# Kernel tuning notes

Measured on AMD Instinct MI355X. Metric: run time of the kernel, lower is better.

The kernel has to match this reference:

```python
import jax, jax.numpy as jnp
import numpy as np

N_NODES = 50000
N_EDGES = 800000
D_IN = 128
H1 = H2 = H3 = 128
N_CLASS = 16
N_GRAPHS = 500


def setup_inputs() -> dict:
    key = jax.random.key(0)
    ks = jax.random.split(key, 10)
    x = jax.random.normal(ks[0], (N_NODES, D_IN), dtype=jnp.float32)
    edge_src = jax.random.randint(ks[1], (N_EDGES,), 0, N_NODES)
    edge_dst = jax.random.randint(ks[2], (N_EDGES,), 0, N_NODES)
    idx = jnp.sort(jax.random.randint(ks[3], (N_NODES,), 0, N_GRAPHS))
    s = 0.02  # small init scale
    W1 = jax.random.normal(ks[4], (D_IN, H1), dtype=jnp.float32) * s
    W2 = jax.random.normal(ks[5], (H1, H2), dtype=jnp.float32) * s
    W3 = jax.random.normal(ks[6], (H2, H3), dtype=jnp.float32) * s
    W4 = jax.random.normal(ks[7], (H3, N_CLASS), dtype=jnp.float32) * s
    b1 = jnp.zeros((H1,), jnp.float32)
    b2 = jnp.zeros((H2,), jnp.float32)
    b3 = jnp.zeros((H3,), jnp.float32)
    b4 = jnp.zeros((N_CLASS,), jnp.float32)
    return {"x": x, "edge_src": edge_src, "edge_dst": edge_dst, "idx": idx,
            "W1": W1, "b1": b1, "W2": W2, "b2": b2,
            "W3": W3, "b3": b3, "W4": W4, "b4": b4}


def reference(x, edge_src, edge_dst, idx, W1, b1, W2, b2, W3, b3, W4, b4):
    # adj_tilde @ h  with binary adjacency + identity, in edge-list form:
    # row i accumulates h[j] for every edge (i<-j), plus h[i] from the eye.
    def propagate(h):
        return h + jax.ops.segment_sum(h[edge_src], edge_dst, num_segments=h.shape[0])

    z1 = jax.nn.relu(propagate(x) @ W1 + b1)            # [N, H1]
    h = propagate(z1) @ W2 + b2                          # [N, H2]
    # scatter_add pooling per graph id (fixed number of graphs for jit)
    pooled = jax.ops.segment_sum(h, idx, num_segments=N_GRAPHS)  # [G, H2]
    zg = jax.nn.relu(pooled @ W3 + b3)                   # [G, H3]
    out = zg @ W4 + b4                                   # [G, C]
    return jax.nn.log_softmax(out, axis=1)
```

## Files before the change

kernel.cpp:

```cpp
#include <hip/hip_runtime.h>
#include <hip/hip_bf16.h>
#include <math.h>

#define NN 50000
#define NE 800000
#define DD 128
#define NG 500
#define NC 16

#define BBITS 6
#define BDSTS 64
#define NBK ((NN + BDSTS - 1) / BDSTS)
#define NCHUNK 256
#define EPB (NE / NCHUNK)
#define ECAP 1536
#define NSLICE 4

using short8 = __attribute__((ext_vector_type(8))) short;
using f32x4  = __attribute__((ext_vector_type(4))) float;

static __device__ __forceinline__ ushort f2bf(float f) {
    __hip_bfloat16 h = __float2bfloat16(f);
    ushort r;
    __builtin_memcpy(&r, &h, sizeof(r));
    return r;
}
static __device__ __forceinline__ float bflo(uint v) { return __uint_as_float(v << 16); }
static __device__ __forceinline__ float bfhi(uint v) { return __uint_as_float(v & 0xffff0000u); }
static __device__ __forceinline__ uint packbf(float lo, float hi) {
    return ((uint)f2bf(hi) << 16) | (uint)f2bf(lo);
}

static __device__ __forceinline__ void add8(float* acc, uint4 v) {
    acc[0] += bflo(v.x); acc[1] += bfhi(v.x);
    acc[2] += bflo(v.y); acc[3] += bfhi(v.y);
    acc[4] += bflo(v.z); acc[5] += bfhi(v.z);
    acc[6] += bflo(v.w); acc[7] += bfhi(v.w);
}

static __device__ __forceinline__ int lower_bound_idx(const int* __restrict__ idx, int g) {
    if (g >= NG) return NN;
    int lo = 0, hi = NN;
    while (lo < hi) {
        int mid = (lo + hi) >> 1;
        if (idx[mid] < g) lo = mid + 1; else hi = mid;
    }
    return lo;
}

static __device__ __forceinline__ int chunk_of_block(int blk) {
    return (blk & 7) * 32 + (blk >> 3);
}

__global__ __launch_bounds__(256) void csr_count_kernel(const int* __restrict__ edst,
                                                        int* __restrict__ cnt) {
    __shared__ int hist[NBK];
    int t = threadIdx.x;
    int chunk = chunk_of_block(blockIdx.x);
    const int e0 = chunk * EPB;
    for (int b = t; b < NBK; b += 256) hist[b] = 0;
    __syncthreads();
    for (int i = t; i < EPB; i += 256) atomicAdd(&hist[edst[e0 + i] >> BBITS], 1);
    __syncthreads();
    for (int b = t; b < NBK; b += 256) cnt[(size_t)chunk * NBK + b] = hist[b];
}

__global__ __launch_bounds__(256) void csr_scan1_kernel(const int* __restrict__ cnt,
                                                        int* __restrict__ bpos,
                                                        int* __restrict__ btot) {
    __shared__ int s[256];
    int b = blockIdx.x, t = threadIdx.x;
    int v = cnt[(size_t)t * NBK + b];
    s[t] = v;
    __syncthreads();
    for (int d = 1; d < 256; d <<= 1) {
        int x = (t >= d) ? s[t - d] : 0;
        __syncthreads();
        s[t] += x;
        __syncthreads();
    }
    bpos[b * NCHUNK + t] = s[t] - v;
    if (t == 255) btot[b] = s[255];
}

__global__ __launch_bounds__(1024) void csr_scan2_kernel(const int* __restrict__ btot,
                                                         int* __restrict__ bbase) {
    __shared__ int s[1024];
    int t = threadIdx.x;
    int v = (t < NBK) ? btot[t] : 0;
    s[t] = v;
    __syncthreads();
    for (int d = 1; d < 1024; d <<= 1) {
        int x = (t >= d) ? s[t - d] : 0;
        __syncthreads();
        s[t] += x;
        __syncthreads();
    }
    if (t < NBK) bbase[t] = s[t] - v;
}

__global__ __launch_bounds__(256) void csr_scatter_kernel(const int* __restrict__ esrc,
                                                          const int* __restrict__ edst,
                                                          const int* __restrict__ bbase,
                                                          const int* __restrict__ bpos,
                                                          uint* __restrict__ baux) {
    __shared__ int lbase[NBK];
    __shared__ int cur[NBK];
    int t = threadIdx.x;
    int chunk = chunk_of_block(blockIdx.x);
    const int e0 = chunk * EPB;
    for (int b = t; b < NBK; b += 256) {
        lbase[b] = bbase[b] + bpos[b * NCHUNK + chunk];
        cur[b] = 0;
    }
    __syncthreads();
    for (int i = t; i < EPB; i += 256) {
        int d = edst[e0 + i], s = esrc[e0 + i];
        int b = d >> BBITS;
        int r = atomicAdd(&cur[b], 1);
        baux[lbase[b] + r] = ((uint)(d & (BDSTS - 1)) << 16) | (uint)s;
    }
}

__global__ __launch_bounds__(256) void bucket_sort_kernel(const uint* __restrict__ baux,
                                                          const int* __restrict__ btot,
                                                          const int* __restrict__ bbase,
                                                          int* __restrict__ offsets,
                                                          ushort* __restrict__ csr) {
    __shared__ uint ent[ECAP];
    __shared__ int hist[BDSTS], lofs[BDSTS], cur[BDSTS];
    int b = blockIdx.x, t = threadIdx.x;
    int n = btot[b];
    int base = bbase[b];
    if (t < BDSTS) hist[t] = 0;
    __syncthreads();
    for (int i = t; i < n; i += 256) {
        uint e = baux[base + i];
        ent[i] = e;
        atomicAdd(&hist[e >> 16], 1);
    }
    __syncthreads();
    if (t < BDSTS) lofs[t] = hist[t];
    __syncthreads();
    for (int d = 1; d < BDSTS; d <<= 1) {
        int x = 0;
        if (t < BDSTS && t >= d) x = lofs[t - d];
        __syncthreads();
        if (t < BDSTS) lofs[t] += x;
        __syncthreads();
    }
    int d0 = b * BDSTS;
    if (t < BDSTS) {
        int excl = lofs[t] - hist[t];
        lofs[t] = excl;
        cur[t] = 0;
        if (d0 + t < NN) offsets[d0 + t] = base + excl;
    }
    if (b == NBK - 1 && t == 0) offsets[NN] = NE;
    __syncthreads();
    for (int i = t; i < n; i += 256) {
        uint e = ent[i];
        int j = e >> 16;
        int pos = base + lofs[j] + atomicAdd(&cur[j], 1);
        csr[pos] = (ushort)(e & 0xffffu);
    }
}

__global__ void convert_w1t_kernel(const float* __restrict__ W1, ushort* __restrict__ W1t) {
    int flat = blockIdx.x * 256 + threadIdx.x;
    if (flat < 128 * 128) {
        int k = flat >> 7, n = flat & 127;
        W1t[n * 128 + k] = f2bf(W1[flat]);
    }
}

__global__ __launch_bounds__(256) void gemm_mfma_kernel(const float* __restrict__ X,
                                                        const ushort* __restrict__ W1t,
                                                        ushort* __restrict__ Y, int M) {
    const int tid = threadIdx.x;
    const int wave = tid >> 6, lane = tid & 63;
    const int wm = wave >> 1, wn = wave & 1;
    const int m0 = blockIdx.x * 128 + wm * 64;
    const int n0 = wn * 64;
    const int lr = lane & 15;
    const int lk = (lane >> 4) * 8;

    int rows[4];
    bool valid[4];
    #pragma unroll
    for (int m = 0; m < 4; ++m) {
        rows[m] = m0 + m * 16 + lr;
        valid[m] = rows[m] < M;
    }

    f32x4 acc[4][4] = {};

    #pragma unroll
    for (int kc = 0; kc < 4; ++kc) {
        const int kb = kc * 32 + lk;
        short8 a[4];
        #pragma unroll
        for (int m = 0; m < 4; ++m) {
            union { short8 v; ushort u[8]; } ua;
            if (valid[m]) {
                const float* p = &X[(size_t)rows[m] * 128 + kb];
                float4 v0 = *reinterpret_cast<const float4*>(p);
                float4 v1 = *reinterpret_cast<const float4*>(p + 4);
                ua.u[0] = f2bf(v0.x); ua.u[1] = f2bf(v0.y);
                ua.u[2] = f2bf(v0.z); ua.u[3] = f2bf(v0.w);
                ua.u[4] = f2bf(v1.x); ua.u[5] = f2bf(v1.y);
                ua.u[6] = f2bf(v1.z); ua.u[7] = f2bf(v1.w);
            } else {
                #pragma unroll
                for (int j = 0; j < 8; ++j) ua.u[j] = 0;
            }
            a[m] = ua.v;
        }
        short8 b[4];
        #pragma unroll
        for (int n = 0; n < 4; ++n) {
            b[n] = *reinterpret_cast<const short8*>(&W1t[(size_t)(n0 + n * 16 + lr) * 128 + kb]);
        }
        #pragma unroll
        for (int m = 0; m < 4; ++m)
            #pragma unroll
            for (int n = 0; n < 4; ++n)
                acc[m][n] = __builtin_amdgcn_mfma_f32_16x16x32_bf16(a[m], b[n], acc[m][n], 0, 0, 0);
    }

    const int rbase = (lane >> 4) * 4;
    #pragma unroll
    for (int m = 0; m < 4; ++m) {
        #pragma unroll
        for (int r = 0; r < 4; ++r) {
            int row = m0 + m * 16 + rbase + r;
            if (row < M) {
                #pragma unroll
                for (int n = 0; n < 4; ++n) {
                    Y[(size_t)row * 128 + n0 + n * 16 + lr] = f2bf(acc[m][n][r]);
                }
            }
        }
    }
}

__global__ __launch_bounds__(256) void prop1_kernel(const ushort* __restrict__ In,
                                                    const int* __restrict__ offs,
                                                    const ushort* __restrict__ csr,
                                                    const float* __restrict__ bias,
                                                    ushort* __restrict__ Out, int n) {
    int node = (blockIdx.x * blockDim.x + threadIdx.x) >> 6;
    int lane = threadIdx.x & 63;
    if (node >= n) return;
    const int q = lane >> 4;
    const int p = lane & 15;
    const uint4* Ir = reinterpret_cast<const uint4*>(In);

    float acc[8] = {};
    if (q == 0) add8(acc, Ir[(size_t)node * 16 + p]);

    int e = offs[node] + q, e1 = offs[node + 1];
    for (; e + 12 < e1; e += 16) {
        int s0 = csr[e], s1 = csr[e + 4], s2 = csr[e + 8], s3 = csr[e + 12];
        uint4 v0 = Ir[(size_t)s0 * 16 + p];
        uint4 v1 = Ir[(size_t)s1 * 16 + p];
        uint4 v2 = Ir[(size_t)s2 * 16 + p];
        uint4 v3 = Ir[(size_t)s3 * 16 + p];
        add8(acc, v0); add8(acc, v1); add8(acc, v2); add8(acc, v3);
    }
    for (; e < e1; e += 4) add8(acc, Ir[(size_t)csr[e] * 16 + p]);

    #pragma unroll
    for (int j = 0; j < 8; ++j) {
        acc[j] += __shfl_xor(acc[j], 16);
        acc[j] += __shfl_xor(acc[j], 32);
    }

    if (q == 0) {
        float4 bA = *reinterpret_cast<const float4*>(&bias[p * 8]);
        float4 bB = *reinterpret_cast<const float4*>(&bias[p * 8 + 4]);
        uint4 o;
        o.x = packbf(fmaxf(acc[0] + bA.x, 0.f), fmaxf(acc[1] + bA.y, 0.f));
        o.y = packbf(fmaxf(acc[2] + bA.z, 0.f), fmaxf(acc[3] + bA.w, 0.f));
        o.z = packbf(fmaxf(acc[4] + bB.x, 0.f), fmaxf(acc[5] + bB.y, 0.f));
        o.w = packbf(fmaxf(acc[6] + bB.z, 0.f), fmaxf(acc[7] + bB.w, 0.f));
        reinterpret_cast<uint4*>(Out)[(size_t)node * 16 + p] = o;
    }
}

__global__ __launch_bounds__(256) void prop2pool_kernel(const ushort* __restrict__ Z1,
                                                        const int* __restrict__ offs,
                                                        const ushort* __restrict__ csr,
                                                        const int* __restrict__ idx,
                                                        float* __restrict__ partials) {
    int g = blockIdx.x >> 2, s = blockIdx.x & (NSLICE - 1);
    int gs = lower_bound_idx(idx, g);
    int ge = lower_bound_idx(idx, g + 1);
    int w = threadIdx.x >> 6, lane = threadIdx.x & 63;
    int q = lane >> 4, p = lane & 15;
    int stream = s * 16 + w * 4 + q;
    const uint4* Zr = reinterpret_cast<const uint4*>(Z1);

    float acc[8] = {};
    for (int i = gs + stream; i < ge; i += 64) add8(acc, Zr[(size_t)i * 16 + p]);
    int E0 = offs[gs], E1 = offs[ge];
    int e = E0 + stream;
    for (; e + 64 < E1; e += 128) {
        int s0 = csr[e], s1 = csr[e + 64];
        uint4 v0 = Zr[(size_t)s0 * 16 + p];
        uint4 v1 = Zr[(size_t)s1 * 16 + p];
        add8(acc, v0); add8(acc, v1);
    }
    if (e < E1) add8(acc, Zr[(size_t)csr[e] * 16 + p]);

    #pragma unroll
    for (int j = 0; j < 8; ++j) {
        acc[j] += __shfl_xor(acc[j], 16);
        acc[j] += __shfl_xor(acc[j], 32);
    }
    __shared__ float red[4][128];
    if (q == 0) {
        #pragma unroll
        for (int j = 0; j < 8; ++j) red[w][p * 8 + j] = acc[j];
    }
    __syncthreads();
    int t = threadIdx.x;
    if (t < 128) {
        partials[((size_t)g * NSLICE + s) * 128 + t] =
            red[0][t] + red[1][t] + red[2][t] + red[3][t];
    }
}

__global__ __launch_bounds__(128) void head_kernel(const float* __restrict__ partials,
                                                   const int* __restrict__ idx,
                                                   const float* __restrict__ W2, const float* __restrict__ b2,
                                                   const float* __restrict__ W3, const float* __restrict__ b3,
                                                   const float* __restrict__ W4, const float* __restrict__ b4,
                                                   float* __restrict__ out) {
    int g = blockIdx.x, t = threadIdx.x;
    __shared__ float vs[128], hs[128], zs[128], os[16];
    const float* pp = &partials[(size_t)g * NSLICE * 128];
    vs[t] = pp[t] + pp[128 + t] + pp[256 + t] + pp[384 + t];
    __syncthreads();
    float c = (float)(lower_bound_idx(idx, g + 1) - lower_bound_idx(idx, g));
    float a = c * b2[t];
    #pragma unroll 8
    for (int k = 0; k < 128; ++k) a = fmaf(vs[k], W2[k * 128 + t], a);
    hs[t] = a;
    __syncthreads();
    float z = b3[t];
    #pragma unroll 8
    for (int k = 0; k < 128; ++k) z = fmaf(hs[k], W3[k * 128 + t], z);
    zs[t] = fmaxf(z, 0.f);
    __syncthreads();
    if (t < 16) {
        float oo = b4[t];
        #pragma unroll 8
        for (int k = 0; k < 128; ++k) oo = fmaf(zs[k], W4[k * 16 + t], oo);
        os[t] = oo;
    }
    __syncthreads();
    if (t < 16) {
        float m = -INFINITY;
        #pragma unroll
        for (int k = 0; k < 16; ++k) m = fmaxf(m, os[k]);
        float ssum = 0.f;
        #pragma unroll
        for (int k = 0; k < 16; ++k) ssum += expf(os[k] - m);
        out[g * 16 + t] = os[t] - m - logf(ssum);
    }
}

extern "C" void kernel_launch(void* const* d_in, const int* in_sizes, int n_in,
                              void* d_out, int out_size, void* d_ws, size_t ws_size,
                              hipStream_t stream) {
    const float* x    = (const float*)d_in[0];
    const int*   esrc = (const int*)d_in[1];
    const int*   edst = (const int*)d_in[2];
    const int*   idx  = (const int*)d_in[3];
    const float* W1   = (const float*)d_in[4];
    const float* b1   = (const float*)d_in[5];
    const float* W2   = (const float*)d_in[6];
    const float* b2   = (const float*)d_in[7];
    const float* W3   = (const float*)d_in[8];
    const float* b3   = (const float*)d_in[9];
    const float* W4   = (const float*)d_in[10];
    const float* b4   = (const float*)d_in[11];
    float* out = (float*)d_out;

    char* w = (char*)d_ws;
    auto alloc = [&](size_t bytes) -> void* {
        void* p = (void*)w;
        w += (bytes + 255) & ~(size_t)255;
        return p;
    };
    int* cnt      = (int*)alloc((size_t)NCHUNK * NBK * 4);
    int* bpos     = (int*)alloc((size_t)NBK * NCHUNK * 4);
    int* btot     = (int*)alloc((size_t)NBK * 4);
    int* bbase    = (int*)alloc((size_t)NBK * 4);
    uint* baux    = (uint*)alloc((size_t)NE * 4);
    int* offsets  = (int*)alloc((size_t)(NN + 1) * 4);
    ushort* csr   = (ushort*)alloc((size_t)NE * 2);
    ushort* w1t   = (ushort*)alloc((size_t)DD * DD * 2);
    ushort* y     = (ushort*)alloc((size_t)NN * DD * 2);
    ushort* z1    = (ushort*)alloc((size_t)NN * DD * 2);
    float* partials = (float*)alloc((size_t)NG * NSLICE * DD * 4);

    convert_w1t_kernel<<<64, 256, 0, stream>>>(W1, w1t);

    csr_count_kernel<<<NCHUNK, 256, 0, stream>>>(edst, cnt);
    csr_scan1_kernel<<<NBK, 256, 0, stream>>>(cnt, bpos, btot);
    csr_scan2_kernel<<<1, 1024, 0, stream>>>(btot, bbase);
    csr_scatter_kernel<<<NCHUNK, 256, 0, stream>>>(esrc, edst, bbase, bpos, baux);
    bucket_sort_kernel<<<NBK, 256, 0, stream>>>(baux, btot, bbase, offsets, csr);

    gemm_mfma_kernel<<<(NN + 127) / 128, 256, 0, stream>>>(x, w1t, y, NN);

    prop1_kernel<<<NN / 4, 256, 0, stream>>>(y, offsets, csr, b1, z1, NN);

    prop2pool_kernel<<<NG * NSLICE, 256, 0, stream>>>(z1, offsets, csr, idx, partials);

    head_kernel<<<NG, 128, 0, stream>>>(partials, idx, W2, b2, W3, b3, W4, b4, out);
}
```

Measured before the change: 135.1 us.

## Merge independent setup kernels into shared launches and unroll pooling gather

Independent setup stages now share launches: the W1 transpose/convert runs as extra blocks of the CSR count kernel, and the first GEMM runs as extra blocks of the per-bucket scan kernel. This removes two launches and lets the GEMM overlap with the CSR scan work. Separately, the prop2pool edge gather is unrolled from two to four outstanding loads per stream to raise memory-level parallelism. The cost is heterogeneous blocks in one grid, which can raise register and shared-memory pressure and lower occupancy for the fused kernels.

```diff
diff --git a/kernel.cpp b/kernel.cpp
--- a/kernel.cpp
+++ b/kernel.cpp
@@ -15,6 +15,7 @@
 #define EPB (NE / NCHUNK)
 #define ECAP 1536
 #define NSLICE 4
+#define GEMMBLK ((NN + 127) / 128)
 
 using short8 = __attribute__((ext_vector_type(8))) short;
 using f32x4  = __attribute__((ext_vector_type(4))) float;
@@ -52,135 +53,36 @@
     return (blk & 7) * 32 + (blk >> 3);
 }
 
-__global__ __launch_bounds__(256) void csr_count_kernel(const int* __restrict__ edst,
-                                                        int* __restrict__ cnt) {
-    __shared__ int hist[NBK];
+__global__ __launch_bounds__(256) void k0_count_convert_kernel(const int* __restrict__ edst,
+                                                               int* __restrict__ cnt,
+                                                               const float* __restrict__ W1,
+                                                               ushort* __restrict__ W1t) {
     int t = threadIdx.x;
-    int chunk = chunk_of_block(blockIdx.x);
-    const int e0 = chunk * EPB;
-    for (int b = t; b < NBK; b += 256) hist[b] = 0;
-    __syncthreads();
-    for (int i = t; i < EPB; i += 256) atomicAdd(&hist[edst[e0 + i] >> BBITS], 1);
-    __syncthreads();
-    for (int b = t; b < NBK; b += 256) cnt[(size_t)chunk * NBK + b] = hist[b];
-}
-
-__global__ __launch_bounds__(256) void csr_scan1_kernel(const int* __restrict__ cnt,
-                                                        int* __restrict__ bpos,
-                                                        int* __restrict__ btot) {
-    __shared__ int s[256];
-    int b = blockIdx.x, t = threadIdx.x;
-    int v = cnt[(size_t)t * NBK + b];
-    s[t] = v;
-    __syncthreads();
-    for (int d = 1; d < 256; d <<= 1) {
-        int x = (t >= d) ? s[t - d] : 0;
-        __syncthreads();
-        s[t] += x;
-        __syncthreads();
-    }
-    bpos[b * NCHUNK + t] = s[t] - v;
-    if (t == 255) btot[b] = s[255];
-}
-
-__global__ __launch_bounds__(1024) void csr_scan2_kernel(const int* __restrict__ btot,
-                                                         int* __restrict__ bbase) {
-    __shared__ int s[1024];
-    int t = threadIdx.x;
-    int v = (t < NBK) ? btot[t] : 0;
-    s[t] = v;
-    __syncthreads();
-    for (int d = 1; d < 1024; d <<= 1) {
-        int x = (t >= d) ? s[t - d] : 0;
-        __syncthreads();
-        s[t] += x;
-        __syncthreads();
-    }
-    if (t < NBK) bbase[t] = s[t] - v;
-}
-
-__global__ __launch_bounds__(256) void csr_scatter_kernel(const int* __restrict__ esrc,
-                                                          const int* __restrict__ edst,
-                                                          const int* __restrict__ bbase,
-                                                          const int* __restrict__ bpos,
-                                                          uint* __restrict__ baux) {
-    __shared__ int lbase[NBK];
-    __shared__ int cur[NBK];
-    int t = threadIdx.x;
-    int chunk = chunk_of_block(blockIdx.x);
-    const int e0 = chunk * EPB;
-    for (int b = t; b < NBK; b += 256) {
-        lbase[b] = bbase[b] + bpos[b * NCHUNK + chunk];
-        cur[b] = 0;
-    }
-    __syncthreads();
-    for (int i = t; i < EPB; i += 256) {
-        int d = edst[e0 + i], s = esrc[e0 + i];
-        int b = d >> BBITS;
-        int r = atomicAdd(&cur[b], 1);
-        baux[lbase[b] + r] = ((uint)(d & (BDSTS - 1)) << 16) | (uint)s;
-    }
-}
-
-__global__ __launch_bounds__(256) void bucket_sort_kernel(const uint* __restrict__ baux,
-                                                          const int* __restrict__ btot,
-                                                          const int* __restrict__ bbase,
-                                                          int* __restrict__ offsets,
-                                                          ushort* __restrict__ csr) {
-    __shared__ uint ent[ECAP];
-    __shared__ int hist[BDSTS], lofs[BDSTS], cur[BDSTS];
-    int b = blockIdx.x, t = threadIdx.x;
-    int n = btot[b];
-    int base = bbase[b];
-    if (t < BDSTS) hist[t] = 0;
-    __syncthreads();
-    for (int i = t; i < n; i += 256) {
-        uint e = baux[base + i];
-        ent[i] = e;
-        atomicAdd(&hist[e >> 16], 1);
-    }
-    __syncthreads();
-    if (t < BDSTS) lofs[t] = hist[t];
-    __syncthreads();
-    for (int d = 1; d < BDSTS; d <<= 1) {
-        int x = 0;
-        if (t < BDSTS && t >= d) x = lofs[t - d];
-        __syncthreads();
-        if (t < BDSTS) lofs[t] += x;
-        __syncthreads();
-    }
-    int d0 = b * BDSTS;
-    if (t < BDSTS) {
-        int excl = lofs[t] - hist[t];
-        lofs[t] = excl;
-        cur[t] = 0;
-        if (d0 + t < NN) offsets[d0 + t] = base + excl;
-    }
-    if (b == NBK - 1 && t == 0) offsets[NN] = NE;
-    __syncthreads();
-    for (int i = t; i < n; i += 256) {
-        uint e = ent[i];
-        int j = e >> 16;
-        int pos = base + lofs[j] + atomicAdd(&cur[j], 1);
-        csr[pos] = (ushort)(e & 0xffffu);
-    }
-}
-
-__global__ void convert_w1t_kernel(const float* __restrict__ W1, ushort* __restrict__ W1t) {
-    int flat = blockIdx.x * 256 + threadIdx.x;
-    if (flat < 128 * 128) {
-        int k = flat >> 7, n = flat & 127;
-        W1t[n * 128 + k] = f2bf(W1[flat]);
-    }
-}
-
-__global__ __launch_bounds__(256) void gemm_mfma_kernel(const float* __restrict__ X,
-                                                        const ushort* __restrict__ W1t,
-                                                        ushort* __restrict__ Y, int M) {
-    const int tid = threadIdx.x;
+    if (blockIdx.x < NCHUNK) {
+        __shared__ int hist[NBK];
+        int chunk = chunk_of_block(blockIdx.x);
+        const int e0 = chunk * EPB;
+        for (int b = t; b < NBK; b += 256) hist[b] = 0;
+        __syncthreads();
+        for (int i = t; i < EPB; i += 256) atomicAdd(&hist[edst[e0 + i] >> BBITS], 1);
+        __syncthreads();
+        for (int b = t; b < NBK; b += 256) cnt[(size_t)chunk * NBK + b] = hist[b];
+    } else {
+        int flat = (blockIdx.x - NCHUNK) * 256 + t;
+        if (flat < 128 * 128) {
+            int k = flat >> 7, n = flat & 127;
+            W1t[n * 128 + k] = f2bf(W1[flat]);
+        }
+    }
+}
+
+static __device__ __forceinline__ void gemm_body(int blk, int tid,
+                                                 const float* __restrict__ X,
+                                                 const ushort* __restrict__ W1t,
+                                                 ushort* __restrict__ Y, int M) {
     const int wave = tid >> 6, lane = tid & 63;
     const int wm = wave >> 1, wn = wave & 1;
-    const int m0 = blockIdx.x * 128 + wm * 64;
+    const int m0 = blk * 128 + wm * 64;
     const int n0 = wn * 64;
     const int lr = lane & 15;
     const int lk = (lane >> 4) * 8;
@@ -244,6 +146,114 @@
     }
 }
 
+__global__ __launch_bounds__(256) void k1_gemm_scan1_kernel(const float* __restrict__ X,
+                                                            const ushort* __restrict__ W1t,
+                                                            ushort* __restrict__ Y,
+                                                            const int* __restrict__ cnt,
+                                                            int* __restrict__ bpos,
+                                                            int* __restrict__ btot) {
+    if (blockIdx.x < GEMMBLK) {
+        gemm_body(blockIdx.x, threadIdx.x, X, W1t, Y, NN);
+    } else {
+        __shared__ int s[256];
+        int b = blockIdx.x - GEMMBLK, t = threadIdx.x;
+        int v = cnt[(size_t)t * NBK + b];
+        s[t] = v;
+        __syncthreads();
+        for (int d = 1; d < 256; d <<= 1) {
+            int x = (t >= d) ? s[t - d] : 0;
+            __syncthreads();
+            s[t] += x;
+            __syncthreads();
+        }
+        bpos[b * NCHUNK + t] = s[t] - v;
+        if (t == 255) btot[b] = s[255];
+    }
+}
+
+__global__ __launch_bounds__(1024) void csr_scan2_kernel(const int* __restrict__ btot,
+                                                         int* __restrict__ bbase) {
+    __shared__ int s[1024];
+    int t = threadIdx.x;
+    int v = (t < NBK) ? btot[t] : 0;
+    s[t] = v;
+    __syncthreads();
+    for (int d = 1; d < 1024; d <<= 1) {
+        int x = (t >= d) ? s[t - d] : 0;
+        __syncthreads();
+        s[t] += x;
+        __syncthreads();
+    }
+    if (t < NBK) bbase[t] = s[t] - v;
+}
+
+__global__ __launch_bounds__(256) void csr_scatter_kernel(const int* __restrict__ esrc,
+                                                          const int* __restrict__ edst,
+                                                          const int* __restrict__ bbase,
+                                                          const int* __restrict__ bpos,
+                                                          uint* __restrict__ baux) {
+    __shared__ int lbase[NBK];
+    __shared__ int cur[NBK];
+    int t = threadIdx.x;
+    int chunk = chunk_of_block(blockIdx.x);
+    const int e0 = chunk * EPB;
+    for (int b = t; b < NBK; b += 256) {
+        lbase[b] = bbase[b] + bpos[b * NCHUNK + chunk];
+        cur[b] = 0;
+    }
+    __syncthreads();
+    for (int i = t; i < EPB; i += 256) {
+        int d = edst[e0 + i], s = esrc[e0 + i];
+        int b = d >> BBITS;
+        int r = atomicAdd(&cur[b], 1);
+        baux[lbase[b] + r] = ((uint)(d & (BDSTS - 1)) << 16) | (uint)s;
+    }
+}
+
+__global__ __launch_bounds__(256) void bucket_sort_kernel(const uint* __restrict__ baux,
+                                                          const int* __restrict__ btot,
+                                                          const int* __restrict__ bbase,
+                                                          int* __restrict__ offsets,
+                                                          ushort* __restrict__ csr) {
+    __shared__ uint ent[ECAP];
+    __shared__ int hist[BDSTS], lofs[BDSTS], cur[BDSTS];
+    int b = blockIdx.x, t = threadIdx.x;
+    int n = btot[b];
+    int base = bbase[b];
+    if (t < BDSTS) hist[t] = 0;
+    __syncthreads();
+    for (int i = t; i < n; i += 256) {
+        uint e = baux[base + i];
+        ent[i] = e;
+        atomicAdd(&hist[e >> 16], 1);
+    }
+    __syncthreads();
+    if (t < BDSTS) lofs[t] = hist[t];
+    __syncthreads();
+    for (int d = 1; d < BDSTS; d <<= 1) {
+        int x = 0;
+        if (t < BDSTS && t >= d) x = lofs[t - d];
+        __syncthreads();
+        if (t < BDSTS) lofs[t] += x;
+        __syncthreads();
+    }
+    int d0 = b * BDSTS;
+    if (t < BDSTS) {
+        int excl = lofs[t] - hist[t];
+        lofs[t] = excl;
+        cur[t] = 0;
+        if (d0 + t < NN) offsets[d0 + t] = base + excl;
+    }
+    if (b == NBK - 1 && t == 0) offsets[NN] = NE;
+    __syncthreads();
+    for (int i = t; i < n; i += 256) {
+        uint e = ent[i];
+        int j = e >> 16;
+        int pos = base + lofs[j] + atomicAdd(&cur[j], 1);
+        csr[pos] = (ushort)(e & 0xffffu);
+    }
+}
+
 __global__ __launch_bounds__(256) void prop1_kernel(const ushort* __restrict__ In,
                                                     const int* __restrict__ offs,
                                                     const ushort* __restrict__ csr,
@@ -305,13 +315,15 @@
     for (int i = gs + stream; i < ge; i += 64) add8(acc, Zr[(size_t)i * 16 + p]);
     int E0 = offs[gs], E1 = offs[ge];
     int e = E0 + stream;
-    for (; e + 64 < E1; e += 128) {
-        int s0 = csr[e], s1 = csr[e + 64];
+    for (; e + 192 < E1; e += 256) {
+        int s0 = csr[e], s1 = csr[e + 64], s2 = csr[e + 128], s3 = csr[e + 192];
         uint4 v0 = Zr[(size_t)s0 * 16 + p];
         uint4 v1 = Zr[(size_t)s1 * 16 + p];
-        add8(acc, v0); add8(acc, v1);
-    }
-    if (e < E1) add8(acc, Zr[(size_t)csr[e] * 16 + p]);
+        uint4 v2 = Zr[(size_t)s2 * 16 + p];
+        uint4 v3 = Zr[(size_t)s3 * 16 + p];
+        add8(acc, v0); add8(acc, v1); add8(acc, v2); add8(acc, v3);
+    }
+    for (; e < E1; e += 64) add8(acc, Zr[(size_t)csr[e] * 16 + p]);
 
     #pragma unroll
     for (int j = 0; j < 8; ++j) {
@@ -406,16 +418,14 @@
     ushort* z1    = (ushort*)alloc((size_t)NN * DD * 2);
     float* partials = (float*)alloc((size_t)NG * NSLICE * DD * 4);
 
-    convert_w1t_kernel<<<64, 256, 0, stream>>>(W1, w1t);
-
-    csr_count_kernel<<<NCHUNK, 256, 0, stream>>>(edst, cnt);
-    csr_scan1_kernel<<<NBK, 256, 0, stream>>>(cnt, bpos, btot);
+    k0_count_convert_kernel<<<NCHUNK + 64, 256, 0, stream>>>(edst, cnt, W1, w1t);
+
+    k1_gemm_scan1_kernel<<<GEMMBLK + NBK, 256, 0, stream>>>(x, w1t, y, cnt, bpos, btot);
+
     csr_scan2_kernel<<<1, 1024, 0, stream>>>(btot, bbase);
     csr_scatter_kernel<<<NCHUNK, 256, 0, stream>>>(esrc, edst, bbase, bpos, baux);
     bucket_sort_kernel<<<NBK, 256, 0, stream>>>(baux, btot, bbase, offsets, csr);
 
-    gemm_mfma_kernel<<<(NN + 127) / 128, 256, 0, stream>>>(x, w1t, y, NN);
-
     prop1_kernel<<<NN / 4, 256, 0, stream>>>(y, offsets, csr, b1, z1, NN);
 
     prop2pool_kernel<<<NG * NSLICE, 256, 0, stream>>>(z1, offsets, csr, idx, partials);
```

After: 127.6 us. 5.5% less time.
